# Kernel optimization log

Measured on AMD Instinct MI355X. Metric: run time of the kernel, lower is better.

The kernel has to match this reference:

```python
import jax, jax.numpy as jnp
import numpy as np

# ---- static config (mirrors MonitorRetina init) ----
N, S, H, W = 256, 1, 144, 256        # stimulus: [N, S, H, W]
HR, WR = 144, 256                    # retina height/width
FOV_HALF_RAD = 0.5 * 75.0 * np.pi / 180.0   # Angular retina, degrees=75
GELU_GAMMA = 1.7015043497085571      # variance-preserving gain for gelu
OUT_OF_RANGE = 10.0                  # grid value for rays missing the monitor


def isotropic_grid_2d(h, w):
    """Pixel-center coordinates, isotropic (normalized by max dim), [-1,1] on the long axis."""
    m = float(max(h, w))
    y = (jnp.arange(h, dtype=jnp.float32) * 2.0 + 1.0 - h) / m
    x = (jnp.arange(w, dtype=jnp.float32) * 2.0 + 1.0 - w) / m
    gy, gx = jnp.meshgrid(y, x, indexing="ij")
    return gx, gy  # each [h, w]


def rmat_3d(ax, ay, az):
    """Batched 3D rotation matrix R = Rz @ Ry @ Rx from Euler angles, each [N]."""
    cx, sx = jnp.cos(ax), jnp.sin(ax)
    cy, sy = jnp.cos(ay), jnp.sin(ay)
    cz, sz = jnp.cos(az), jnp.sin(az)
    one, zero = jnp.ones_like(ax), jnp.zeros_like(ax)
    Rx = jnp.stack([one, zero, zero, zero, cx, -sx, zero, sx, cx], -1).reshape(-1, 3, 3)
    Ry = jnp.stack([cy, zero, sy, zero, one, zero, -sy, zero, cy], -1).reshape(-1, 3, 3)
    Rz = jnp.stack([cz, -sz, zero, sz, cz, zero, zero, zero, one], -1).reshape(-1, 3, 3)
    return jnp.einsum("nij,njk,nkl->nil", Rz, Ry, Rx)  # [N,3,3]


def retina_rays(rmat):
    """Angular retina: pixel angles -> unit ray directions, rotated per batch. [N,HR,WR,3]."""
    gx, gy = isotropic_grid_2d(HR, WR)
    ax, ay = gx * FOV_HALF_RAD, gy * FOV_HALF_RAD
    a = jnp.sqrt(ax * ax + ay * ay) + 1e-12
    sinc = jnp.sin(a) / a
    d = jnp.stack([sinc * ax, sinc * ay, jnp.cos(a)], -1)  # [HR,WR,3]
    return jnp.einsum("nij,hwj->nhwi", rmat, d)


def monitor_project(rays):
    """Plane monitor at unit distance along +z: perspective divide to isotropic grid coords. [N,HR,WR,2]."""
    rz = rays[..., 2]
    safe = rz > 1e-3
    inv = jnp.where(safe, rz, 1.0)
    gx = jnp.where(safe, rays[..., 0] / inv, OUT_OF_RANGE)
    gy = jnp.where(safe, rays[..., 1] / inv, OUT_OF_RANGE)
    return jnp.stack([gx, gy], -1)


def isotropic_grid_sample_2d(x, grid, pad_value=0.0):
    """Bilinear sample x:[N,C,H,W] at grid:[N,H',W',2] (isotropic coords), constant padding."""
    m = float(max(H, W))
    px = (grid[..., 0] * m + W - 1.0) * 0.5  # [N,H',W'] pixel coords
    py = (grid[..., 1] * m + H - 1.0) * 0.5
    x0 = jnp.floor(px)
    y0 = jnp.floor(py)
    wx = px - x0
    wy = py - y0
    x0i = x0.astype(jnp.int32)
    y0i = y0.astype(jnp.int32)

    def corner(img, yi, xi):
        valid = (xi >= 0) & (xi < W) & (yi >= 0) & (yi < H)
        v = img[:, jnp.clip(yi, 0, H - 1), jnp.clip(xi, 0, W - 1)]  # [C,H',W']
        return jnp.where(valid[None], v, pad_value)

    def one(img, y0i, x0i, wx, wy):
        v00 = corner(img, y0i, x0i)
        v01 = corner(img, y0i, x0i + 1)
        v10 = corner(img, y0i + 1, x0i)
        v11 = corner(img, y0i + 1, x0i + 1)
        return (v00 * (1 - wx) + v01 * wx) * (1 - wy) + (v10 * (1 - wx) + v11 * wx) * wy

    return jax.vmap(one)(x, y0i, x0i, wx, wy)  # [N,C,H',W']


def setup_inputs() -> dict:
    key = jax.random.key(0)
    ks = jax.random.split(key, 8)
    F, D = 16, 128
    return {
        "stimulus": jax.random.normal(ks[0], (N, S, H, W), jnp.float32),
        "perspective": jax.random.normal(ks[1], (N, F), jnp.float32),
        "W1": jax.random.normal(ks[2], (F, D), jnp.float32) / np.sqrt(F),
        "b1": jnp.zeros((D,), jnp.float32),
        "W2": jax.random.normal(ks[3], (D, D), jnp.float32) / np.sqrt(D),
        "b2": jnp.zeros((D,), jnp.float32),
        "Wp": jax.random.normal(ks[4], (D, 3), jnp.float32) * 0.05,  # proj gains init near 0
        "bp": jnp.zeros((3,), jnp.float32),
    }


def reference(stimulus, perspective, W1, b1, W2, b2, Wp, bp):
    # MLP -> 3 angles -> rotation matrix (rmat)
    h = jax.nn.gelu(perspective @ W1 + b1) * GELU_GAMMA
    h = jax.nn.gelu(h @ W2 + b2) * GELU_GAMMA
    ang = h @ Wp + bp                      # [N,3]
    rm = rmat_3d(ang[:, 0], ang[:, 1], ang[:, 2])
    rays = retina_rays(rm)                 # [N,HR,WR,3]
    grid = monitor_project(rays)           # [N,HR,WR,2]
    # monitor_pixel / retina_pixel are Raw (identity) transforms
    return isotropic_grid_sample_2d(stimulus, grid, pad_value=0.0)  # [N,S,HR,WR]
```

## Files before the change

### kernel.cpp

```cpp
#include <hip/hip_runtime.h>
#include <math.h>

#define NB    256
#define IMG_H 144
#define IMG_W 256
#define IMG_ELEMS (IMG_H * IMG_W)
#define FDIM  16
#define DDIM  128

#define STRIDE 260
#define SROWS  76
#define SIMG_FLOATS (SROWS * STRIDE)

#define FOV_HALF_RAD 0.6544984694978736f
#define GELU_GAMMA   1.7015043497085571f

typedef float f32x4 __attribute__((ext_vector_type(4)));
typedef const __attribute__((address_space(1))) unsigned int glb_u32;
typedef __attribute__((address_space(3))) unsigned int lds_u32;

__device__ __forceinline__ float gelu_gamma(float x) {
    const float k0 = 0.7978845608028654f;
    const float k1 = 0.044715f;
    float t = tanhf(k0 * (x + k1 * x * x * x));
    return 0.5f * x * (1.0f + t) * GELU_GAMMA;
}

__global__ void __launch_bounds__(1024, 8) fused_retina_kernel(
    const float* __restrict__ stim,
    const float* __restrict__ persp,
    const float* __restrict__ W1,
    const float* __restrict__ b1,
    const float* __restrict__ W2,
    const float* __restrict__ b2,
    const float* __restrict__ Wp,
    const float* __restrict__ bp,
    float* __restrict__ out)
{
    __shared__ float simg[SIMG_FLOATS];
    __shared__ float sh1[DDIM];
    __shared__ float sR[9];

    const int tid  = threadIdx.x;
    const int bid  = blockIdx.x;
    const int n    = bid >> 1;
    const int half = bid & 1;
    const int wid  = tid >> 6;
    const int lane = tid & 63;

    const float* __restrict__ img = stim + (size_t)n * IMG_ELEMS;

    {
        const int nzr = half ? 4 : 3;
        f32x4 z = {0.0f, 0.0f, 0.0f, 0.0f};
        if (tid < nzr * 65) {
            const int zi = tid / 65;
            const int g  = tid - zi * 65;
            int row;
            if (half) row = (zi == 0) ? 0 : (72 + zi);
            else      row = (zi == 0) ? 0 : (73 + zi);
            *(f32x4*)&simg[row * STRIDE + g * 4] = z;
        } else {
            const int t     = tid - nzr * 65;
            const int nleft = half ? 72 : 73;
            if (t < nleft)
                *(f32x4*)&simg[(t + 1) * STRIDE] = z;
        }
    }

    const int row0  = half ? 72 : 0;
    const int nrows = half ? 72 : 73;

    if (wid > 0) {
        const int v = wid - 1;
#pragma unroll
        for (int p = 0; p < 5; ++p) {
            const int j = v + 15 * p;
            if (j < nrows) {
                const float* gsrc = img + (size_t)(row0 + j) * IMG_W + lane * 4;
                float* ldst = &simg[(j + 1) * STRIDE + 4];
                __builtin_amdgcn_global_load_lds(
                    (glb_u32*)gsrc, (lds_u32*)ldst, 16, 0, 0);
            }
        }
    } else {
        float a0 = b1[lane], a1 = b1[lane + 64];
#pragma unroll
        for (int f = 0; f < FDIM; ++f) {
            const float p = persp[n * FDIM + f];
            a0 = fmaf(p, W1[f * DDIM + lane],      a0);
            a1 = fmaf(p, W1[f * DDIM + lane + 64], a1);
        }
        sh1[lane]      = gelu_gamma(a0);
        sh1[lane + 64] = gelu_gamma(a1);
        asm volatile("s_waitcnt lgkmcnt(0)" ::: "memory");

        float c0 = b2[lane], c1 = b2[lane + 64];
#pragma unroll 8
        for (int k = 0; k < DDIM; ++k) {
            const float s = sh1[k];
            c0 = fmaf(s, W2[k * DDIM + lane],      c0);
            c1 = fmaf(s, W2[k * DDIM + lane + 64], c1);
        }
        const float g0 = gelu_gamma(c0);
        const float g1 = gelu_gamma(c1);

        float p0 = fmaf(g0, Wp[lane * 3 + 0], g1 * Wp[(lane + 64) * 3 + 0]);
        float p1 = fmaf(g0, Wp[lane * 3 + 1], g1 * Wp[(lane + 64) * 3 + 1]);
        float p2 = fmaf(g0, Wp[lane * 3 + 2], g1 * Wp[(lane + 64) * 3 + 2]);
#pragma unroll
        for (int m = 32; m >= 1; m >>= 1) {
            p0 += __shfl_xor(p0, m);
            p1 += __shfl_xor(p1, m);
            p2 += __shfl_xor(p2, m);
        }

        if (lane == 0) {
            const float ax = p0 + bp[0], ay = p1 + bp[1], az = p2 + bp[2];
            const float cx = cosf(ax), sx = sinf(ax);
            const float cy = cosf(ay), sy = sinf(ay);
            const float cz = cosf(az), sz = sinf(az);
            sR[0] = cz * cy;  sR[1] = cz * sy * sx - sz * cx;  sR[2] = cz * sy * cx + sz * sx;
            sR[3] = sz * cy;  sR[4] = sz * sy * sx + cz * cx;  sR[5] = sz * sy * cx - cz * sx;
            sR[6] = -sy;      sR[7] = cy * sx;                 sR[8] = cy * cx;
        }
    }
    __syncthreads();

    const float r0 = sR[0], r1 = sR[1], r2 = sR[2];
    const float r3 = sR[3], r4 = sR[4], r5 = sR[5];
    const float r6 = sR[6], r7 = sR[7], r8 = sR[8];

    float* __restrict__ outn = out + (size_t)n * IMG_ELEMS;

    const int w     = tid & 255;
    const int hbase = tid >> 8;
    const float gx  = ((float)(2 * w + 1) - 256.0f) * (1.0f / 256.0f);
    const float axv = gx * FOV_HALF_RAD;
    const float ax2 = axv * axv;
    const float A0 = r0 * axv, A1 = r3 * axv, A2 = r6 * axv;
    const int sb = half ? 71 : -1;

#pragma unroll 4
    for (int it = 0; it < 36; ++it) {
        const int h   = it * 4 + hbase;
        const int px0 = (h << 8) | w;

        const float gy  = ((float)(2 * h + 1) - 144.0f) * (1.0f / 256.0f);
        const float ayv = gy * FOV_HALF_RAD;
        const float tt  = fmaf(ayv, ayv, ax2);

        float sc = fmaf(tt, 2.7557319e-6f, -1.9841270e-4f);
        sc = fmaf(tt, sc,  8.3333333e-3f);
        sc = fmaf(tt, sc, -1.6666667e-1f);
        sc = fmaf(tt, sc,  1.0f);

        float ca = fmaf(tt, 2.4801587e-5f, -1.3888889e-3f);
        ca = fmaf(tt, ca,  4.1666667e-2f);
        ca = fmaf(tt, ca, -0.5f);
        ca = fmaf(tt, ca,  1.0f);

        const float rx = fmaf(sc, fmaf(r1, ayv, A0), r2 * ca);
        const float ry = fmaf(sc, fmaf(r4, ayv, A1), r5 * ca);
        const float rz = fmaf(sc, fmaf(r7, ayv, A2), r8 * ca);

        const float inv  = __builtin_amdgcn_rcpf(rz);
        const float s128 = 128.0f * inv;
        const bool  safe = rz > 0.001f;

        float pxf = fmaf(rx, s128, 127.5f);
        float pyf = fmaf(ry, s128, 71.5f);
        pxf = safe ? pxf : 300.0f;
        pyf = safe ? pyf : 300.0f;
        pxf = fminf(fmaxf(pxf, -1.0f), 256.0f);
        pyf = fminf(fmaxf(pyf, -1.0f), 144.0f);

        const float x0f = floorf(pxf), y0f = floorf(pyf);
        const float wx  = pxf - x0f,   wy  = pyf - y0f;
        const int   xi  = (int)x0f,    yi  = (int)y0f;

        const bool mine = half ? (yi >= 72) : (yi <= 71);
        const int  a00  = mine ? ((yi - sb) * STRIDE + xi + 4) : 4;
        const int  a10  = a00 + STRIDE;

        const float v00 = simg[a00];
        const float v01 = simg[a00 + 1];
        const float v10 = simg[a10];
        const float v11 = simg[a10 + 1];

        const float top = fmaf(wx, v01 - v00, v00);
        const float bot = fmaf(wx, v11 - v10, v10);
        const float res = fmaf(wy, bot - top, top);

        if (mine)
            __builtin_nontemporal_store(res, outn + px0);
    }
}

extern "C" void kernel_launch(void* const* d_in, const int* in_sizes, int n_in,
                              void* d_out, int out_size, void* d_ws, size_t ws_size,
                              hipStream_t stream) {
    const float* stimulus    = (const float*)d_in[0];
    const float* perspective = (const float*)d_in[1];
    const float* W1          = (const float*)d_in[2];
    const float* b1          = (const float*)d_in[3];
    const float* W2          = (const float*)d_in[4];
    const float* b2          = (const float*)d_in[5];
    const float* Wp          = (const float*)d_in[6];
    const float* bp          = (const float*)d_in[7];
    float* out = (float*)d_out;

    (void)d_ws; (void)ws_size;

    fused_retina_kernel<<<NB * 2, 1024, 0, stream>>>(
        stimulus, perspective, W1, b1, W2, b2, Wp, bp, out);
}
```

Baseline: 117.8 us.

## Replace LDS image staging with L2-prefetched direct global gathers and XCD swizzle

Removes the per-block LDS copy of half the stimulus image and instead has the non-MLP warps read the whole image through ordinary loads. The values are discarded; the loads only exist to pull the image into cache while warp 0 runs the MLP. The bilinear sample then gathers its four taps straight from global memory with bounds masks. Each block now handles only its own output rows, so the duplicated 'mine' filtering goes away. Block indices are remapped so both halves of an image land on the same XCD and share L2. This drops the 79KB LDS footprint and the redundant work, at the cost of scattered global gathers that depend on cache hits.

```diff
diff --git a/kernel.cpp b/kernel.cpp
--- a/kernel.cpp
+++ b/kernel.cpp
@@ -8,16 +8,11 @@
 #define FDIM  16
 #define DDIM  128
 
-#define STRIDE 260
-#define SROWS  76
-#define SIMG_FLOATS (SROWS * STRIDE)
-
 #define FOV_HALF_RAD 0.6544984694978736f
 #define GELU_GAMMA   1.7015043497085571f
+#define OUT_OF_RANGE 10.0f
 
 typedef float f32x4 __attribute__((ext_vector_type(4)));
-typedef const __attribute__((address_space(1))) unsigned int glb_u32;
-typedef __attribute__((address_space(3))) unsigned int lds_u32;
 
 __device__ __forceinline__ float gelu_gamma(float x) {
     const float k0 = 0.7978845608028654f;
@@ -37,52 +32,32 @@
     const float* __restrict__ bp,
     float* __restrict__ out)
 {
-    __shared__ float simg[SIMG_FLOATS];
     __shared__ float sh1[DDIM];
     __shared__ float sR[9];
 
     const int tid  = threadIdx.x;
-    const int bid  = blockIdx.x;
-    const int n    = bid >> 1;
-    const int half = bid & 1;
+    const int hw   = blockIdx.x;
+    const int lg   = (hw & 7) * 64 + (hw >> 3);
+    const int n    = lg >> 1;
+    const int half = lg & 1;
     const int wid  = tid >> 6;
     const int lane = tid & 63;
 
     const float* __restrict__ img = stim + (size_t)n * IMG_ELEMS;
 
-    {
-        const int nzr = half ? 4 : 3;
-        f32x4 z = {0.0f, 0.0f, 0.0f, 0.0f};
-        if (tid < nzr * 65) {
-            const int zi = tid / 65;
-            const int g  = tid - zi * 65;
-            int row;
-            if (half) row = (zi == 0) ? 0 : (72 + zi);
-            else      row = (zi == 0) ? 0 : (73 + zi);
-            *(f32x4*)&simg[row * STRIDE + g * 4] = z;
-        } else {
-            const int t     = tid - nzr * 65;
-            const int nleft = half ? 72 : 73;
-            if (t < nleft)
-                *(f32x4*)&simg[(t + 1) * STRIDE] = z;
-        }
-    }
-
-    const int row0  = half ? 72 : 0;
-    const int nrows = half ? 72 : 73;
-
     if (wid > 0) {
-        const int v = wid - 1;
+        const int t = tid - 64;
+        const f32x4* __restrict__ src = (const f32x4*)img;
+        float acc = 0.0f;
 #pragma unroll
-        for (int p = 0; p < 5; ++p) {
-            const int j = v + 15 * p;
-            if (j < nrows) {
-                const float* gsrc = img + (size_t)(row0 + j) * IMG_W + lane * 4;
-                float* ldst = &simg[(j + 1) * STRIDE + 4];
-                __builtin_amdgcn_global_load_lds(
-                    (glb_u32*)gsrc, (lds_u32*)ldst, 16, 0, 0);
+        for (int p = 0; p < 10; ++p) {
+            const int g = t + p * 960;
+            if (g < 9216) {
+                f32x4 v = src[g];
+                acc += v[0] + v[1] + v[2] + v[3];
             }
         }
+        asm volatile("" :: "v"(acc));
     } else {
         float a0 = b1[lane], a1 = b1[lane + 64];
 #pragma unroll
@@ -134,15 +109,14 @@
     float* __restrict__ outn = out + (size_t)n * IMG_ELEMS;
 
     const int w     = tid & 255;
-    const int hbase = tid >> 8;
+    const int hbase = (tid >> 8) + half * 72;
     const float gx  = ((float)(2 * w + 1) - 256.0f) * (1.0f / 256.0f);
     const float axv = gx * FOV_HALF_RAD;
     const float ax2 = axv * axv;
     const float A0 = r0 * axv, A1 = r3 * axv, A2 = r6 * axv;
-    const int sb = half ? 71 : -1;
 
-#pragma unroll 4
-    for (int it = 0; it < 36; ++it) {
+#pragma unroll 3
+    for (int it = 0; it < 18; ++it) {
         const int h   = it * 4 + hbase;
         const int px0 = (h << 8) | w;
 
@@ -165,35 +139,43 @@
         const float rz = fmaf(sc, fmaf(r7, ayv, A2), r8 * ca);
 
         const float inv  = __builtin_amdgcn_rcpf(rz);
-        const float s128 = 128.0f * inv;
         const bool  safe = rz > 0.001f;
+        const float gxp  = safe ? rx * inv : OUT_OF_RANGE;
+        const float gyp  = safe ? ry * inv : OUT_OF_RANGE;
 
-        float pxf = fmaf(rx, s128, 127.5f);
-        float pyf = fmaf(ry, s128, 71.5f);
-        pxf = safe ? pxf : 300.0f;
-        pyf = safe ? pyf : 300.0f;
-        pxf = fminf(fmaxf(pxf, -1.0f), 256.0f);
-        pyf = fminf(fmaxf(pyf, -1.0f), 144.0f);
+        const float pxf = fmaf(gxp, 128.0f, 127.5f);
+        const float pyf = fmaf(gyp, 128.0f, 71.5f);
 
         const float x0f = floorf(pxf), y0f = floorf(pyf);
         const float wx  = pxf - x0f,   wy  = pyf - y0f;
-        const int   xi  = (int)x0f,    yi  = (int)y0f;
+        const int   x0  = (int)x0f,    y0  = (int)y0f;
+        const int   x1  = x0 + 1,      y1  = y0 + 1;
 
-        const bool mine = half ? (yi >= 72) : (yi <= 71);
-        const int  a00  = mine ? ((yi - sb) * STRIDE + xi + 4) : 4;
-        const int  a10  = a00 + STRIDE;
+        const bool vx0 = (unsigned)x0 < IMG_W;
+        const bool vx1 = (unsigned)x1 < IMG_W;
+        const bool vy0 = (unsigned)y0 < IMG_H;
+        const bool vy1 = (unsigned)y1 < IMG_H;
 
-        const float v00 = simg[a00];
-        const float v01 = simg[a00 + 1];
-        const float v10 = simg[a10];
-        const float v11 = simg[a10 + 1];
+        const int xc0 = min(max(x0, 0), IMG_W - 1);
+        const int xc1 = min(max(x1, 0), IMG_W - 1);
+        const int yb0 = min(max(y0, 0), IMG_H - 1) << 8;
+        const int yb1 = min(max(y1, 0), IMG_H - 1) << 8;
 
-        const float top = fmaf(wx, v01 - v00, v00);
-        const float bot = fmaf(wx, v11 - v10, v10);
+        const float l00 = img[yb0 + xc0];
+        const float l01 = img[yb0 + xc1];
+        const float l10 = img[yb1 + xc0];
+        const float l11 = img[yb1 + xc1];
+
+        const float c00 = (vx0 & vy0) ? l00 : 0.0f;
+        const float c01 = (vx1 & vy0) ? l01 : 0.0f;
+        const float c10 = (vx0 & vy1) ? l10 : 0.0f;
+        const float c11 = (vx1 & vy1) ? l11 : 0.0f;
+
+        const float top = fmaf(wx, c01 - c00, c00);
+        const float bot = fmaf(wx, c11 - c10, c10);
         const float res = fmaf(wy, bot - top, top);
 
-        if (mine)
-            __builtin_nontemporal_store(res, outn + px0);
+        __builtin_nontemporal_store(res, outn + px0);
     }
 }
 
```

Measured after the change: 140.4 us. 1.19x slower.
